# Kernel tuning notes

Measured on AMD Instinct MI355X. Metric: run time of the kernel, lower is better.

Reference implementation:

```python
import jax, jax.numpy as jnp
import numpy as np

B, H, W = 64, 512, 512
TOP_K = 200
N_OBJS = 200
KP_THRES = 0.1
IOU_THR = 0.5
RESIZE_H, RESIZE_W = 512.0, 512.0


def setup_inputs() -> dict:
    key = jax.random.key(0)
    k1, k2, k3 = jax.random.split(key, 3)
    heatmap_y = jax.random.uniform(k1, (B, H), dtype=jnp.float32)
    heatmap_x = jax.random.uniform(k2, (B, W), dtype=jnp.float32)
    # box sizes in heatmap pixels (scaled so boxes are non-degenerate)
    size_maps = jax.random.uniform(k3, (B, H, W, 2), dtype=jnp.float32) * 64.0
    origin_shapes = jnp.full((B, 2), 1024.0, dtype=jnp.float32)
    return {"heatmap_y": heatmap_y, "heatmap_x": heatmap_x,
            "size_maps": size_maps, "origin_shapes": origin_shapes}


def _iou_one_vs_all(box, boxes):
    # box: (4,) [y1,x1,y2,x2]; boxes: (N,4)
    yy1 = jnp.maximum(box[0], boxes[:, 0])
    xx1 = jnp.maximum(box[1], boxes[:, 1])
    yy2 = jnp.minimum(box[2], boxes[:, 2])
    xx2 = jnp.minimum(box[3], boxes[:, 3])
    inter = jnp.maximum(yy2 - yy1, 0.0) * jnp.maximum(xx2 - xx1, 0.0)
    a1 = (box[2] - box[0]) * (box[3] - box[1])
    a2 = (boxes[:, 2] - boxes[:, 0]) * (boxes[:, 3] - boxes[:, 1])
    denom = a1 + a2 - inter
    return jnp.where(denom > 0.0, inter / jnp.maximum(denom, 1e-12), 0.0)


def _nms_single(boxes, scores):
    # greedy NMS over N boxes, selecting up to N_OBJS (TF combined_non_max_suppression,
    # single class, clip_boxes=False, score_threshold=-inf, zero-padded output)
    N = boxes.shape[0]

    def body(i, st):
        active, sb, ss, cnt = st
        ms = jnp.where(active, scores, -jnp.inf)
        j = jnp.argmax(ms)
        valid = ms[j] > -jnp.inf
        bj = boxes[j]
        ious = _iou_one_vs_all(bj, boxes)
        active = active & (ious <= IOU_THR)
        active = active.at[j].set(False)
        sb = sb.at[i].set(jnp.where(valid, bj, jnp.zeros_like(bj)))
        ss = ss.at[i].set(jnp.where(valid, scores[j], 0.0))
        return (active, sb, ss, cnt + valid.astype(jnp.int32))

    init = (jnp.ones((N,), dtype=bool),
            jnp.zeros((N_OBJS, 4), boxes.dtype),
            jnp.zeros((N_OBJS,), scores.dtype),
            jnp.array(0, jnp.int32))
    _, sb, ss, cnt = jax.lax.fori_loop(0, N_OBJS, body, init)
    return sb, ss, cnt


def _decode(heatmap_y, heatmap_x, size_maps, origin_shapes):
    Bd, Hd = heatmap_y.shape
    Wd = heatmap_x.shape[1]
    # rank-1 heatmap: matmul(hy[...,None], hx[...,None]^T) == outer product -> (B,H,W)
    hm = heatmap_y[:, :, None] * heatmap_x[:, None, :]
    # 3x3 max-pool peak suppression (CenterNet keep-mask)
    hmax = jax.lax.reduce_window(hm, -jnp.inf, jax.lax.max,
                                 (1, 3, 3), (1, 1, 1), 'SAME')
    hm = jnp.where(hmax == hm, hm, 0.0)
    # top-k over flattened spatial dims (c == 1)
    scores, idx = jax.lax.top_k(hm.reshape(Bd, Hd * Wd), TOP_K)  # (B,K)
    ys = idx // Wd
    xs = idx % Wd
    bidx = jnp.arange(Bd)[:, None]
    sizes = size_maps[bidx, ys, xs]                      # (B,K,2) gather_nd
    centers = jnp.stack([ys, xs], axis=-1).astype(hm.dtype)  # (B,K,2)
    tls = jnp.maximum(centers - sizes / 2.0, 0.0)        # clamp tl at 0
    brs = centers + sizes / 2.0
    br_y = jnp.minimum(brs[..., 0], RESIZE_H - 1.0)
    br_x = jnp.minimum(brs[..., 1], RESIZE_W - 1.0)
    # resize back to original image coords
    ratio = origin_shapes / jnp.asarray([RESIZE_H, RESIZE_W], dtype=hm.dtype)  # (B,2)
    ry = ratio[:, 0:1]
    rx = ratio[:, 1:2]
    boxes = jnp.stack([tls[..., 0] * ry, tls[..., 1] * rx,
                       br_y * ry, br_x * rx], axis=-1)   # (B,K,4)
    # threshold mask + scatter into -1-initialized output (indices == own positions)
    mask = scores > KP_THRES
    boxes = jnp.where(mask[..., None], boxes, -1.0)
    sc = jnp.where(mask, scores, -1.0)
    if TOP_K < N_OBJS:
        boxes = jnp.pad(boxes, ((0, 0), (0, N_OBJS - TOP_K), (0, 0)), constant_values=-1.0)
        sc = jnp.pad(sc, ((0, 0), (0, N_OBJS - TOP_K)), constant_values=-1.0)
    nb, ns, _cnt = jax.vmap(_nms_single)(boxes, sc)      # (B,N_OBJS,4), (B,N_OBJS)
    # post: -1 boxes -> inf, 0 (NMS padding) boxes -> inf
    nb = jnp.where(nb == -1.0, jnp.inf, nb)
    nb = jnp.where(nb == 0.0, jnp.inf, nb)
    classes = jnp.zeros_like(ns)                         # single class -> class id 0
    out = jnp.concatenate([nb, ns[..., None], classes[..., None]], axis=-1)
    return out.reshape(-1, N_OBJS, 6)


def reference(heatmap_y, heatmap_x, size_maps, origin_shapes):
    return _decode(heatmap_y, heatmap_x, size_maps, origin_shapes)
```

## Files before the change

### kernel.cpp

```cpp
#include <hip/hip_runtime.h>
#include <stdint.h>

#define NT 1024
#define HW 512
#define TOPK 200
#define STAIR_GEN 256
#define STAIR_T 204
#define MAXCAND 1024
#define MAXCLOSE 320

typedef unsigned long long u64;
typedef unsigned u32;

__global__ __launch_bounds__(NT, 4) void decode_nms_kernel(
    const float* __restrict__ hyg, const float* __restrict__ hxg,
    const float* __restrict__ size_maps, const float* __restrict__ origin,
    float* __restrict__ out)
{
#pragma clang fp contract(off)
  const int b = blockIdx.x;
  const int tid = threadIdx.x;

  __shared__ __align__(16) float hy[HW];
  __shared__ __align__(16) float hx[HW];
  __shared__ int   cyI[MAXCLOSE + 8], cxI[MAXCLOSE + 8];
  __shared__ __align__(16) float cyV[MAXCLOSE + 8], cyM[MAXCLOSE + 8];
  __shared__ __align__(16) float cxV[MAXCLOSE + 8], cxM[MAXCLOSE + 8];
  __shared__ __align__(16) u64 pK[2][HW + 2];
  __shared__ float sV[2][HW];
  __shared__ int   sI[2][HW];
  __shared__ __align__(16) u64 cand[MAXCAND + 2];
  __shared__ float tS[TOPK];
  __shared__ float4 bb4[256];
  __shared__ __align__(16) float aB[256];
  __shared__ __align__(16) u64 sup[256][4];
  __shared__ int   pickL[TOPK];
  __shared__ int   nCY, nCX, nPk0, nPk1, nCand, survSh;
  __shared__ u32   Tbits;

  if (tid == 0) { nCY = 0; nCX = 0; nPk0 = 0; nPk1 = 0; nCand = 0; Tbits = 0; }

  float ry = origin[b * 2 + 0] / 512.0f;
  float rx = origin[b * 2 + 1] / 512.0f;

  if (tid < 128) {
    ((float4*)hy)[tid] = ((const float4*)(hyg + (size_t)b * HW))[tid];
  } else if (tid < 256) {
    ((float4*)hx)[tid - 128] = ((const float4*)(hxg + (size_t)b * HW))[tid - 128];
  }
  for (int i = tid; i < HW + 2; i += NT) { pK[0][i] = 0ull; pK[1][i] = 0ull; }
  for (int i = tid; i <= MAXCAND; i += NT) cand[i] = 0ull;
  for (int i = tid; i < MAXCLOSE + 8; i += NT) { cxV[i] = 0.f; cxM[i] = 0.f; }
  if (tid < 256) { bb4[tid] = make_float4(0.f, 0.f, 0.f, 0.f); aB[tid] = 0.f; }
  __syncthreads();

  if (tid < HW) {
    int i = tid;
    float v = hy[i], m = v;
    if (i > 0)      m = fmaxf(m, hy[i - 1]);
    if (i < HW - 1) m = fmaxf(m, hy[i + 1]);
    if (v >= m * (1.0f - 1e-6f)) {
      int p = atomicAdd(&nCY, 1);
      if (p < MAXCLOSE) { cyI[p] = i; cyV[p] = v; cyM[p] = m; }
    }
    if (v == m) {
      int p = atomicAdd(&nPk0, 1);
      pK[0][p] = ((u64)__float_as_uint(v) << 32) | (u64)(0xFFFFFFFFu - (u32)i);
    }
  } else {
    int i = tid - HW;
    float w = hx[i], mw = w;
    if (i > 0)      mw = fmaxf(mw, hx[i - 1]);
    if (i < HW - 1) mw = fmaxf(mw, hx[i + 1]);
    if (w >= mw * (1.0f - 1e-6f)) {
      int p = atomicAdd(&nCX, 1);
      if (p < MAXCLOSE) { cxI[p] = i; cxV[p] = w; cxM[p] = mw; }
    }
    if (w == mw) {
      int p = atomicAdd(&nPk1, 1);
      pK[1][p] = ((u64)__float_as_uint(w) << 32) | (u64)(0xFFFFFFFFu - (u32)i);
    }
  }
  __syncthreads();

  int NP0 = nPk0, NP1 = nPk1;
  int ncy = nCY < MAXCLOSE ? nCY : MAXCLOSE;
  int ncx = nCX < MAXCLOSE ? nCX : MAXCLOSE;

  {
    int d = tid >> 9;
    int t = tid & 511;
    int n = d ? NP1 : NP0;
    int n2 = (n + 1) >> 1;
    const ulonglong2* pk2 = (const ulonglong2*)&pK[d][0];
    for (int i = t; i < n; i += 512) {
      u64 key = pK[d][i];
      int rank = 0;
      int j2 = 0;
      for (; j2 + 16 <= n2; j2 += 16) {
        ulonglong2 a0 = pk2[j2+0],  a1 = pk2[j2+1],  a2 = pk2[j2+2],  a3 = pk2[j2+3];
        ulonglong2 a4 = pk2[j2+4],  a5 = pk2[j2+5],  a6 = pk2[j2+6],  a7 = pk2[j2+7];
        ulonglong2 a8 = pk2[j2+8],  a9 = pk2[j2+9],  aA = pk2[j2+10], aB2 = pk2[j2+11];
        ulonglong2 aC = pk2[j2+12], aD = pk2[j2+13], aE = pk2[j2+14], aF = pk2[j2+15];
        rank += (a0.x > key) + (a0.y > key) + (a1.x > key) + (a1.y > key)
              + (a2.x > key) + (a2.y > key) + (a3.x > key) + (a3.y > key)
              + (a4.x > key) + (a4.y > key) + (a5.x > key) + (a5.y > key)
              + (a6.x > key) + (a6.y > key) + (a7.x > key) + (a7.y > key)
              + (a8.x > key) + (a8.y > key) + (a9.x > key) + (a9.y > key)
              + (aA.x > key) + (aA.y > key) + (aB2.x > key) + (aB2.y > key)
              + (aC.x > key) + (aC.y > key) + (aD.x > key) + (aD.y > key)
              + (aE.x > key) + (aE.y > key) + (aF.x > key) + (aF.y > key);
      }
      for (; j2 + 8 <= n2; j2 += 8) {
        ulonglong2 a0 = pk2[j2+0], a1 = pk2[j2+1], a2 = pk2[j2+2], a3 = pk2[j2+3];
        ulonglong2 a4 = pk2[j2+4], a5 = pk2[j2+5], a6 = pk2[j2+6], a7 = pk2[j2+7];
        rank += (a0.x > key) + (a0.y > key) + (a1.x > key) + (a1.y > key)
              + (a2.x > key) + (a2.y > key) + (a3.x > key) + (a3.y > key)
              + (a4.x > key) + (a4.y > key) + (a5.x > key) + (a5.y > key)
              + (a6.x > key) + (a6.y > key) + (a7.x > key) + (a7.y > key);
      }
      for (; j2 < n2; ++j2) {
        ulonglong2 a = pk2[j2];
        rank += (a.x > key) + (a.y > key);
      }
      sV[d][rank] = __uint_as_float((u32)(key >> 32));
      sI[d][rank] = (int)(0xFFFFFFFFu - (u32)(key & 0xFFFFFFFFu));
    }
  }
  __syncthreads();

  {
    int a = tid + 1;
    if (a <= STAIR_T && a <= NP0) {
      int bn = (STAIR_T + a - 1) / a;
      if (bn <= NP1) atomicMax(&Tbits, __float_as_uint(sV[0][a - 1] * sV[1][bn - 1]));
    }
  }
  __syncthreads();
  const float T = __uint_as_float(Tbits);

  {
    int NY = NP0 < STAIR_GEN ? NP0 : STAIR_GEN;
    if (tid < 256) {
      int i = tid >> 4, jc = tid & 15;
      if (i < NY) {
        int jmax = STAIR_GEN / (i + 1); if (jmax > NP1) jmax = NP1;
        int jlo = jc * 16, jhi = jlo + 16; if (jhi > jmax) jhi = jmax;
        float vy = sV[0][i]; int ybase = sI[0][i] * HW;
        #pragma unroll 4
        for (int j = jlo; j < jhi; ++j) {
          float s = vy * sV[1][j];
          if (s > 0.1f && s >= T) {
            int pos = atomicAdd(&nCand, 1);
            if (pos < MAXCAND)
              cand[pos] = ((u64)__float_as_uint(s) << 32)
                        | (u64)(0xFFFFFFFFu - (u32)(ybase + sI[1][j]));
          }
        }
      }
    } else if (tid < 768) {
      int u = tid - 256;
      int i2 = 16 + (u >> 1), c = u & 1;
      if (i2 < NY) {
        int jmax = STAIR_GEN / (i2 + 1); if (jmax > NP1) jmax = NP1;
        int jlo = c * 8, jhi = jlo + 8; if (jhi > jmax) jhi = jmax;
        float vy = sV[0][i2]; int ybase = sI[0][i2] * HW;
        #pragma unroll 4
        for (int j = jlo; j < jhi; ++j) {
          float s = vy * sV[1][j];
          if (s > 0.1f && s >= T) {
            int pos = atomicAdd(&nCand, 1);
            if (pos < MAXCAND)
              cand[pos] = ((u64)__float_as_uint(s) << 32)
                        | (u64)(0xFFFFFFFFu - (u32)(ybase + sI[1][j]));
          }
        }
      }
    } else {
      for (int yi = tid - 768; yi < ncy; yi += 256) {
        float vy = cyV[yi], mvy = cyM[yi];
        bool py = (vy == mvy);
        int ybase = cyI[yi] * HW;
        const float4* cv4 = (const float4*)cxV;
        const float4* cm4 = (const float4*)cxM;
        int nb = (ncx + 7) >> 3;
        for (int blk = 0; blk < nb; ++blk) {
          float4 v0 = cv4[2*blk], v1 = cv4[2*blk + 1];
          float4 m0 = cm4[2*blk], m1 = cm4[2*blk + 1];
          float vv[8] = {v0.x, v0.y, v0.z, v0.w, v1.x, v1.y, v1.z, v1.w};
          float mm[8] = {m0.x, m0.y, m0.z, m0.w, m1.x, m1.y, m1.z, m1.w};
          unsigned hits = 0;
          #pragma unroll
          for (int u8 = 0; u8 < 8; ++u8) {
            float pr = vy * vv[u8];
            bool h = (!(py && vv[u8] == mm[u8])) && (pr == mvy * mm[u8])
                   && (pr > 0.1f) && (pr >= T);
            hits |= ((unsigned)h) << u8;
          }
          if (__builtin_expect(hits != 0, 0)) {
            for (int u8 = 0; u8 < 8; ++u8) if ((hits >> u8) & 1u) {
              int xi = blk * 8 + u8;
              float pr = vy * cxV[xi];
              int pos = atomicAdd(&nCand, 1);
              if (pos < MAXCAND)
                cand[pos] = ((u64)__float_as_uint(pr) << 32)
                          | (u64)(0xFFFFFFFFu - (u32)(ybase + cxI[xi]));
            }
          }
        }
      }
    }
  }
  __syncthreads();
  int C = nCand < MAXCAND ? nCand : MAXCAND;

  {
    int C2 = (C + 1) >> 1;
    const ulonglong2* cd2 = (const ulonglong2*)&cand[0];
    for (int i = tid; i < C; i += NT) {
      u64 k = cand[i];
      int rank = 0;
      int j2 = 0;
      for (; j2 + 16 <= C2; j2 += 16) {
        ulonglong2 a0 = cd2[j2+0],  a1 = cd2[j2+1],  a2 = cd2[j2+2],  a3 = cd2[j2+3];
        ulonglong2 a4 = cd2[j2+4],  a5 = cd2[j2+5],  a6 = cd2[j2+6],  a7 = cd2[j2+7];
        ulonglong2 a8 = cd2[j2+8],  a9 = cd2[j2+9],  aA = cd2[j2+10], aB2 = cd2[j2+11];
        ulonglong2 aC = cd2[j2+12], aD = cd2[j2+13], aE = cd2[j2+14], aF = cd2[j2+15];
        rank += (a0.x > k) + (a0.y > k) + (a1.x > k) + (a1.y > k)
              + (a2.x > k) + (a2.y > k) + (a3.x > k) + (a3.y > k)
              + (a4.x > k) + (a4.y > k) + (a5.x > k) + (a5.y > k)
              + (a6.x > k) + (a6.y > k) + (a7.x > k) + (a7.y > k)
              + (a8.x > k) + (a8.y > k) + (a9.x > k) + (a9.y > k)
              + (aA.x > k) + (aA.y > k) + (aB2.x > k) + (aB2.y > k)
              + (aC.x > k) + (aC.y > k) + (aD.x > k) + (aD.y > k)
              + (aE.x > k) + (aE.y > k) + (aF.x > k) + (aF.y > k);
      }
      for (; j2 + 8 <= C2; j2 += 8) {
        ulonglong2 a0 = cd2[j2+0], a1 = cd2[j2+1], a2 = cd2[j2+2], a3 = cd2[j2+3];
        ulonglong2 a4 = cd2[j2+4], a5 = cd2[j2+5], a6 = cd2[j2+6], a7 = cd2[j2+7];
        rank += (a0.x > k) + (a0.y > k) + (a1.x > k) + (a1.y > k)
              + (a2.x > k) + (a2.y > k) + (a3.x > k) + (a3.y > k)
              + (a4.x > k) + (a4.y > k) + (a5.x > k) + (a5.y > k)
              + (a6.x > k) + (a6.y > k) + (a7.x > k) + (a7.y > k);
      }
      for (; j2 < C2; ++j2) {
        ulonglong2 a = cd2[j2];
        rank += (a.x > k) + (a.y > k);
      }
      if (rank < TOPK) {
        float sc = __uint_as_float((u32)(k >> 32));
        int lin = (int)(0xFFFFFFFFu - (u32)(k & 0xFFFFFFFFu));
        tS[rank] = sc;
        int y = lin >> 9, x = lin & (HW - 1);
        const float* sp = size_maps + (((size_t)b * HW + y) * HW + x) * 2;
        float s0 = sp[0], s1 = sp[1];
        float cy = (float)y, cx = (float)x;
        float b0 = fmaxf(cy - s0 * 0.5f, 0.0f) * ry;
        float b1 = fmaxf(cx - s1 * 0.5f, 0.0f) * rx;
        float b2 = fminf(cy + s0 * 0.5f, 511.0f) * ry;
        float b3 = fminf(cx + s1 * 0.5f, 511.0f) * rx;
        bb4[rank] = make_float4(b0, b1, b2, b3);
        aB[rank] = (b2 - b0) * (b3 - b1);
      }
    }
  }
  __syncthreads();
  int R = C < TOPK ? C : TOPK;

  {
    int k = tid & 255, w = tid >> 8;
    bool hasK = (k < R);
    float4 bk = bb4[k];
    float k0 = bk.x, k1 = bk.y, k2 = bk.z, k3 = bk.w;
    float a1 = (k2 - k0) * (k3 - k1);
    int wv = k >> 6;
    u64 word = 0;
    int jbase = w << 6;
    if (jbase < R && w >= wv) {
      const float4* aB4 = (const float4*)aB;
      for (int jj = 0; jj < 64; jj += 4) {
        float4 bjv[4] = {bb4[jbase+jj], bb4[jbase+jj+1],
                         bb4[jbase+jj+2], bb4[jbase+jj+3]};
        float4 av = aB4[(jbase + jj) >> 2];
        float aarr[4] = {av.x, av.y, av.z, av.w};
        unsigned close = 0;
        u64 wbits = 0;
        #pragma unroll
        for (int u = 0; u < 4; ++u) {
          int j = jbase + jj + u;
          float4 bj = bjv[u];
          float yy1 = fmaxf(k0, bj.x), xx1 = fmaxf(k1, bj.y);
          float yy2 = fminf(k2, bj.z), xx2 = fminf(k3, bj.w);
          float inter = fmaxf(yy2 - yy1, 0.0f) * fmaxf(xx2 - xx1, 0.0f);
          float denom = a1 + aarr[u] - inter;
          float diff = inter - 0.5f * denom;
          bool nearb = (denom > 0.0f) & (fabsf(diff) <= 1e-6f * denom);
          close |= (unsigned)nearb;
          bool s = hasK && (j > k) && (j < R) && (denom > 0.0f) && (diff > 0.0f);
          wbits |= ((u64)s) << (jj + u);
        }
        if (__builtin_expect(__any((int)close), 0)) {
          wbits = 0;
          #pragma unroll
          for (int u = 0; u < 4; ++u) {
            int j = jbase + jj + u;
            float4 bj = bjv[u];
            float yy1 = fmaxf(k0, bj.x), xx1 = fmaxf(k1, bj.y);
            float yy2 = fminf(k2, bj.z), xx2 = fminf(k3, bj.w);
            float inter = fmaxf(yy2 - yy1, 0.0f) * fmaxf(xx2 - xx1, 0.0f);
            float denom = a1 + aarr[u] - inter;
            float iou = (denom > 0.0f) ? (inter / fmaxf(denom, 1e-12f)) : 0.0f;
            bool s = hasK && (j > k) && (j < R) && (iou > 0.5f);
            wbits |= ((u64)s) << (jj + u);
          }
        }
        word |= wbits;
      }
    }
    sup[k][w] = word;
  }
  __syncthreads();

  if (tid == 0) {
    u64 al0 = ~0ull, al1 = ~0ull, al2 = ~0ull, al3 = ~0ull;
    u64 cur[4][4], nxt[4][4];
    #pragma unroll
    for (int t = 0; t < 4; ++t) {
      cur[t][0] = sup[t][0]; cur[t][1] = sup[t][1];
      cur[t][2] = sup[t][2]; cur[t][3] = sup[t][3];
    }
    int s = 0;
    for (int k0 = 0; k0 < R; k0 += 4) {
      #pragma unroll
      for (int t = 0; t < 4; ++t) {
        nxt[t][0] = sup[k0 + 4 + t][0]; nxt[t][1] = sup[k0 + 4 + t][1];
        nxt[t][2] = sup[k0 + 4 + t][2]; nxt[t][3] = sup[k0 + 4 + t][3];
      }
      #pragma unroll
      for (int t = 0; t < 4; ++t) {
        int k = k0 + t;
        if (k < R) {
          u64 aw = (k < 64) ? al0 : (k < 128) ? al1 : (k < 192) ? al2 : al3;
          if ((aw >> (k & 63)) & 1ull) {
            pickL[s++] = k;
            al0 &= ~cur[t][0]; al1 &= ~cur[t][1];
            al2 &= ~cur[t][2]; al3 &= ~cur[t][3];
          }
        }
      }
      #pragma unroll
      for (int t = 0; t < 4; ++t) {
        cur[t][0] = nxt[t][0]; cur[t][1] = nxt[t][1];
        cur[t][2] = nxt[t][2]; cur[t][3] = nxt[t][3];
      }
    }
    survSh = s;
  }
  __syncthreads();

  int surv = survSh;
  int nNeg = TOPK - R;
  for (int r = tid; r < TOPK; r += NT) {
    float o0, o1, o2, o3, o4;
    if (r < surv) {
      int k = pickL[r];
      float4 bk = bb4[k];
      o0 = bk.x; o1 = bk.y; o2 = bk.z; o3 = bk.w; o4 = tS[k];
    } else if (r < surv + nNeg) {
      o0 = o1 = o2 = o3 = -1.0f; o4 = -1.0f;
    } else {
      o0 = o1 = o2 = o3 = 0.0f; o4 = 0.0f;
    }
    float2* o2p = (float2*)(out + ((size_t)b * TOPK + r) * 6);
    o2p[0] = make_float2(o0, o1);
    o2p[1] = make_float2(o2, o3);
    o2p[2] = make_float2(o4, 0.0f);
  }
}

extern "C" void kernel_launch(void* const* d_in, const int* in_sizes, int n_in,
                              void* d_out, int out_size, void* d_ws, size_t ws_size,
                              hipStream_t stream) {
  const float* hyg = (const float*)d_in[0];
  const float* hxg = (const float*)d_in[1];
  const float* szm = (const float*)d_in[2];
  const float* org = (const float*)d_in[3];
  int B = in_sizes[0] / HW;
  decode_nms_kernel<<<dim3(B), dim3(NT), 0, stream>>>(hyg, hxg, szm, org, (float*)d_out);
}
```

Baseline: 223.3 us.

## Early-exit rank counting, trim IoU loop tail, skip loads for suppressed rows in NMS scan

The candidate rank loop now breaks out once a candidate's rank reaches TOP_K, so losing candidates stop scanning early. The pairwise IoU loop stops at the valid box count instead of always doing 64 columns. The serial greedy scan masks the alive bits to R up front, double-buffers with ping-pong A/B buffers, and only loads suppression rows for boxes that are still alive. Together these cut per-candidate compare work and the single-thread scan latency, at the cost of more branching and divergence.

Result: no change. 225.4 us (+0.9%).

```diff
diff --git a/kernel.cpp b/kernel.cpp
--- a/kernel.cpp
+++ b/kernel.cpp
@@ -234,18 +234,21 @@
               + (aA.x > k) + (aA.y > k) + (aB2.x > k) + (aB2.y > k)
               + (aC.x > k) + (aC.y > k) + (aD.x > k) + (aD.y > k)
               + (aE.x > k) + (aE.y > k) + (aF.x > k) + (aF.y > k);
-      }
-      for (; j2 + 8 <= C2; j2 += 8) {
-        ulonglong2 a0 = cd2[j2+0], a1 = cd2[j2+1], a2 = cd2[j2+2], a3 = cd2[j2+3];
-        ulonglong2 a4 = cd2[j2+4], a5 = cd2[j2+5], a6 = cd2[j2+6], a7 = cd2[j2+7];
-        rank += (a0.x > k) + (a0.y > k) + (a1.x > k) + (a1.y > k)
-              + (a2.x > k) + (a2.y > k) + (a3.x > k) + (a3.y > k)
-              + (a4.x > k) + (a4.y > k) + (a5.x > k) + (a5.y > k)
-              + (a6.x > k) + (a6.y > k) + (a7.x > k) + (a7.y > k);
-      }
-      for (; j2 < C2; ++j2) {
-        ulonglong2 a = cd2[j2];
-        rank += (a.x > k) + (a.y > k);
+        if (rank >= TOPK) break;
+      }
+      if (rank < TOPK) {
+        for (; j2 + 8 <= C2; j2 += 8) {
+          ulonglong2 a0 = cd2[j2+0], a1 = cd2[j2+1], a2 = cd2[j2+2], a3 = cd2[j2+3];
+          ulonglong2 a4 = cd2[j2+4], a5 = cd2[j2+5], a6 = cd2[j2+6], a7 = cd2[j2+7];
+          rank += (a0.x > k) + (a0.y > k) + (a1.x > k) + (a1.y > k)
+                + (a2.x > k) + (a2.y > k) + (a3.x > k) + (a3.y > k)
+                + (a4.x > k) + (a4.y > k) + (a5.x > k) + (a5.y > k)
+                + (a6.x > k) + (a6.y > k) + (a7.x > k) + (a7.y > k);
+        }
+        for (; j2 < C2; ++j2) {
+          ulonglong2 a = cd2[j2];
+          rank += (a.x > k) + (a.y > k);
+        }
       }
       if (rank < TOPK) {
         float sc = __uint_as_float((u32)(k >> 32));
@@ -277,8 +280,10 @@
     u64 word = 0;
     int jbase = w << 6;
     if (jbase < R && w >= wv) {
+      int rem = R - jbase;
+      int jhi = rem >= 64 ? 64 : ((rem + 3) & ~3);
       const float4* aB4 = (const float4*)aB;
-      for (int jj = 0; jj < 64; jj += 4) {
+      for (int jj = 0; jj < jhi; jj += 4) {
         float4 bjv[4] = {bb4[jbase+jj], bb4[jbase+jj+1],
                          bb4[jbase+jj+2], bb4[jbase+jj+3]};
         float4 av = aB4[(jbase + jj) >> 2];
@@ -322,36 +327,77 @@
   __syncthreads();
 
   if (tid == 0) {
-    u64 al0 = ~0ull, al1 = ~0ull, al2 = ~0ull, al3 = ~0ull;
-    u64 cur[4][4], nxt[4][4];
+    u64 al0, al1, al2, al3;
+    {
+      int r = R;
+      al0 = (r >= 64) ? ~0ull : ((r <= 0) ? 0ull : ((1ull << r) - 1)); r -= 64;
+      al1 = (r >= 64) ? ~0ull : ((r <= 0) ? 0ull : ((1ull << r) - 1)); r -= 64;
+      al2 = (r >= 64) ? ~0ull : ((r <= 0) ? 0ull : ((1ull << r) - 1)); r -= 64;
+      al3 = (r >= 64) ? ~0ull : ((r <= 0) ? 0ull : ((1ull << r) - 1));
+    }
+    u64 bufA[4][4], bufB[4][4];
     #pragma unroll
     for (int t = 0; t < 4; ++t) {
-      cur[t][0] = sup[t][0]; cur[t][1] = sup[t][1];
-      cur[t][2] = sup[t][2]; cur[t][3] = sup[t][3];
+      const ulonglong2* sp = (const ulonglong2*)&sup[t][0];
+      ulonglong2 r0 = sp[0], r1 = sp[1];
+      bufA[t][0] = r0.x; bufA[t][1] = r0.y; bufA[t][2] = r1.x; bufA[t][3] = r1.y;
     }
     int s = 0;
-    for (int k0 = 0; k0 < R; k0 += 4) {
-      #pragma unroll
-      for (int t = 0; t < 4; ++t) {
-        nxt[t][0] = sup[k0 + 4 + t][0]; nxt[t][1] = sup[k0 + 4 + t][1];
-        nxt[t][2] = sup[k0 + 4 + t][2]; nxt[t][3] = sup[k0 + 4 + t][3];
-      }
-      #pragma unroll
-      for (int t = 0; t < 4; ++t) {
-        int k = k0 + t;
-        if (k < R) {
-          u64 aw = (k < 64) ? al0 : (k < 128) ? al1 : (k < 192) ? al2 : al3;
-          if ((aw >> (k & 63)) & 1ull) {
-            pickL[s++] = k;
-            al0 &= ~cur[t][0]; al1 &= ~cur[t][1];
-            al2 &= ~cur[t][2]; al3 &= ~cur[t][3];
-          }
-        }
-      }
-      #pragma unroll
-      for (int t = 0; t < 4; ++t) {
-        cur[t][0] = nxt[t][0]; cur[t][1] = nxt[t][1];
-        cur[t][2] = nxt[t][2]; cur[t][3] = nxt[t][3];
+    int k0 = 0;
+    for (;;) {
+      {
+        int nb = k0 + 4;
+        u64 naw = (nb < 64) ? al0 : (nb < 128) ? al1 : (nb < 192) ? al2 : al3;
+        unsigned nib = (unsigned)((naw >> (nb & 63)) & 0xFull);
+        if (nib) {
+          #pragma unroll
+          for (int t = 0; t < 4; ++t) if ((nib >> t) & 1u) {
+            const ulonglong2* sp = (const ulonglong2*)&sup[nb + t][0];
+            ulonglong2 r0 = sp[0], r1 = sp[1];
+            bufB[t][0] = r0.x; bufB[t][1] = r0.y; bufB[t][2] = r1.x; bufB[t][3] = r1.y;
+          }
+        }
+        #pragma unroll
+        for (int t = 0; t < 4; ++t) {
+          int k = k0 + t;
+          if (k < R) {
+            u64 aw = (k < 64) ? al0 : (k < 128) ? al1 : (k < 192) ? al2 : al3;
+            if ((aw >> (k & 63)) & 1ull) {
+              pickL[s++] = k;
+              al0 &= ~bufA[t][0]; al1 &= ~bufA[t][1];
+              al2 &= ~bufA[t][2]; al3 &= ~bufA[t][3];
+            }
+          }
+        }
+        k0 += 4;
+        if (k0 >= R) break;
+      }
+      {
+        int nb = k0 + 4;
+        u64 naw = (nb < 64) ? al0 : (nb < 128) ? al1 : (nb < 192) ? al2 : al3;
+        unsigned nib = (unsigned)((naw >> (nb & 63)) & 0xFull);
+        if (nib) {
+          #pragma unroll
+          for (int t = 0; t < 4; ++t) if ((nib >> t) & 1u) {
+            const ulonglong2* sp = (const ulonglong2*)&sup[nb + t][0];
+            ulonglong2 r0 = sp[0], r1 = sp[1];
+            bufA[t][0] = r0.x; bufA[t][1] = r0.y; bufA[t][2] = r1.x; bufA[t][3] = r1.y;
+          }
+        }
+        #pragma unroll
+        for (int t = 0; t < 4; ++t) {
+          int k = k0 + t;
+          if (k < R) {
+            u64 aw = (k < 64) ? al0 : (k < 128) ? al1 : (k < 192) ? al2 : al3;
+            if ((aw >> (k & 63)) & 1ull) {
+              pickL[s++] = k;
+              al0 &= ~bufB[t][0]; al1 &= ~bufB[t][1];
+              al2 &= ~bufB[t][2]; al3 &= ~bufB[t][3];
+            }
+          }
+        }
+        k0 += 4;
+        if (k0 >= R) break;
       }
     }
     survSh = s;
```
